# Performance work log

Measured on AMD Instinct MI355X. Metric: run time of the kernel, lower is better.

Reference implementation:

```python
import jax, jax.numpy as jnp
import numpy as np

N_NODES = 50000
N_EDGES = 800000
N_FEAT = 128
D_HID = 128
N_CLASS = 40


def gcn_conv(x, W, b, src, dst, n_nodes):
    """PyG GCNConv: h = D^{-1/2} (A + I) D^{-1/2} (x @ W) + b.
    src/dst are int arrays [E]; self-loops handled analytically."""
    h = x @ W  # [N, D]
    ones = jnp.ones(src.shape[0], dtype=h.dtype)
    # degree after adding self-loops: 1 + in-degree (edge weights are 1)
    deg = 1.0 + jax.ops.segment_sum(ones, dst, num_segments=n_nodes)
    dinv = jax.lax.rsqrt(deg)  # [N]
    # messages along edges src -> dst with symmetric normalization
    msg = h[src] * (dinv[src] * dinv[dst])[:, None]  # [E, D]
    agg = jax.ops.segment_sum(msg, dst, num_segments=n_nodes)  # [N, D]
    # self-loop contribution: dinv[i]^2 * h[i]
    agg = agg + h * (dinv * dinv)[:, None]
    return agg + b


def setup_inputs() -> dict:
    key = jax.random.key(0)
    ks = jax.random.split(key, 5)
    x = jax.random.normal(ks[0], (N_NODES, N_FEAT), dtype=jnp.float32)
    edge_index = jax.random.randint(ks[1], (2, N_EDGES), 0, N_NODES, dtype=jnp.int64)
    s_in = 1.0 / np.sqrt(N_FEAT)
    s_h = 1.0 / np.sqrt(D_HID)
    W_in = jax.random.normal(ks[2], (N_FEAT, D_HID), dtype=jnp.float32) * s_in
    W1 = jax.random.normal(ks[3], (D_HID, D_HID), dtype=jnp.float32) * s_h
    W_out = jax.random.normal(ks[4], (D_HID, N_CLASS), dtype=jnp.float32) * s_h
    return {
        "x": x,
        "edge_index": edge_index,
        "W_in": W_in,
        "b_in": jnp.zeros((D_HID,), jnp.float32),
        "W1": W1,
        "b1": jnp.zeros((D_HID,), jnp.float32),
        "W_out": W_out,
        "b_out": jnp.zeros((N_CLASS,), jnp.float32),
    }


def reference(x, edge_index, W_in, b_in, W1, b1, W_out, b_out):
    src, dst = edge_index[0], edge_index[1]
    n = x.shape[0]
    # input GCNConv (no activation on input_fc, matching the torch forward)
    h = gcn_conv(x, W_in, b_in, src, dst, n)
    # hidden layer: dropout is identity at eval; relu after conv; normalize=False
    h = jax.nn.relu(gcn_conv(h, W1, b1, src, dst, n))
    out = h @ W_out + b_out
    return jax.nn.log_softmax(out, axis=1)
```

## Files before the change

### kernel.cpp

```cpp
#include <hip/hip_runtime.h>
#include <math.h>


#define THREADS 256

typedef __attribute__((ext_vector_type(8))) short short8v;
typedef __attribute__((ext_vector_type(4))) float float4v;

__device__ __forceinline__ float b2f(unsigned int lo16) {
    return __uint_as_float(lo16 << 16);
}
__device__ __forceinline__ unsigned short f2b(float f) {
    unsigned int u = __float_as_uint(f);
    u += 0x7FFFu + ((u >> 16) & 1u);
    return (unsigned short)(u >> 16);
}

__global__ void detect_idx64(const int* __restrict__ idx, int* __restrict__ flag) {
    int t = threadIdx.x;
    unsigned long long b = __ballot(idx[2 * t + 1] == 0);
    if (t == 0) *flag = (b == 0xFFFFFFFFFFFFFFFFull) ? 1 : 0;
}

__global__ void fill_pos(const int* __restrict__ idx, const int* __restrict__ flag,
                         int* __restrict__ cnt, unsigned int* __restrict__ rec, int E) {
    int e = blockIdx.x * blockDim.x + threadIdx.x;
    if (e >= E) return;
    int f = *flag;
    int src, dst;
    if (f) { src = idx[2 * e]; dst = idx[2 * (E + e)]; }
    else   { src = idx[e];     dst = idx[E + e]; }
    unsigned int pos = (unsigned int)atomicAdd(&cnt[dst], 1);
    rec[e] = ((unsigned int)src << 16) | (pos & 0xFFFFu);
}

__global__ __launch_bounds__(256) void scanA(const int* __restrict__ cnt,
                                             int* __restrict__ bsum, int N) {
    __shared__ int wt[4];
    int tid = threadIdx.x, lane = tid & 63, w = tid >> 6;
    int i = blockIdx.x * 256 + tid;
    int v = (i < N) ? cnt[i] : 0;
    int s = v;
#pragma unroll
    for (int off = 1; off < 64; off <<= 1) {
        int t = __shfl_up(s, off);
        if (lane >= off) s += t;
    }
    if (lane == 63) wt[w] = s;
    __syncthreads();
    if (tid == 0) bsum[blockIdx.x] = wt[0] + wt[1] + wt[2] + wt[3];
}

__global__ __launch_bounds__(256) void scanB(int* __restrict__ bsum,
                                             int* __restrict__ boff,
                                             int* __restrict__ rowstart,
                                             int nb, int N) {
    __shared__ int wt[4];
    __shared__ int wo[5];
    int tid = threadIdx.x, lane = tid & 63, w = tid >> 6;
    int v = (tid < nb) ? bsum[tid] : 0;
    int s = v;
#pragma unroll
    for (int off = 1; off < 64; off <<= 1) {
        int t = __shfl_up(s, off);
        if (lane >= off) s += t;
    }
    if (lane == 63) wt[w] = s;
    __syncthreads();
    if (tid == 0) {
        int run = 0;
#pragma unroll
        for (int k = 0; k < 4; ++k) { wo[k] = run; run += wt[k]; }
        wo[4] = run;
    }
    __syncthreads();
    if (tid < nb) boff[tid] = wo[w] + s - v;
    if (tid == 0) rowstart[N] = wo[4];
}

__global__ __launch_bounds__(256) void scanC(const int* __restrict__ cnt,
                                             const int* __restrict__ boff,
                                             int* __restrict__ rowstart,
                                             float* __restrict__ dinv, int N) {
    __shared__ int wt[4];
    __shared__ int wo[4];
    int tid = threadIdx.x, lane = tid & 63, w = tid >> 6;
    int i = blockIdx.x * 256 + tid;
    int v = (i < N) ? cnt[i] : 0;
    int s = v;
#pragma unroll
    for (int off = 1; off < 64; off <<= 1) {
        int t = __shfl_up(s, off);
        if (lane >= off) s += t;
    }
    if (lane == 63) wt[w] = s;
    __syncthreads();
    if (tid == 0) {
        int run = 0;
#pragma unroll
        for (int k = 0; k < 4; ++k) { wo[k] = run; run += wt[k]; }
    }
    __syncthreads();
    if (i < N) {
        rowstart[i] = boff[blockIdx.x] + wo[w] + (s - v);
        dinv[i] = rsqrtf(1.0f + (float)v);
    }
}

__global__ void fill_place(const int* __restrict__ idx, const int* __restrict__ flag,
                           const unsigned int* __restrict__ rec,
                           const int* __restrict__ rowstart,
                           unsigned short* __restrict__ srcs, int E) {
    int e = blockIdx.x * blockDim.x + threadIdx.x;
    if (e >= E) return;
    int f = *flag;
    int dst = f ? idx[2 * (E + e)] : idx[E + e];
    unsigned int r = rec[e];
    srcs[rowstart[dst] + (int)(r & 0xFFFFu)] = (unsigned short)(r >> 16);
}

__global__ __launch_bounds__(256) void pack_w2(const float* __restrict__ W0,
                                               const float* __restrict__ W1,
                                               uint4* __restrict__ wpk0,
                                               uint4* __restrict__ wpk1) {
    const float* W = blockIdx.x ? W1 : W0;
    uint4* wpk = blockIdx.x ? wpk1 : wpk0;
    int tid = threadIdx.x;
    for (int it = 0; it < 8; ++it) {
        int s = it * 256 + tid;
        int ct = s >> 8;
        int kb = (s >> 6) & 3;
        int l  = s & 63;
        int col = ct * 16 + (l & 15);
        int k0  = kb * 32 + ((l >> 4) << 3);
        unsigned short e0 = f2b(W[(k0 + 0) * 128 + col]);
        unsigned short e1 = f2b(W[(k0 + 1) * 128 + col]);
        unsigned short e2 = f2b(W[(k0 + 2) * 128 + col]);
        unsigned short e3 = f2b(W[(k0 + 3) * 128 + col]);
        unsigned short e4 = f2b(W[(k0 + 4) * 128 + col]);
        unsigned short e5 = f2b(W[(k0 + 5) * 128 + col]);
        unsigned short e6 = f2b(W[(k0 + 6) * 128 + col]);
        unsigned short e7 = f2b(W[(k0 + 7) * 128 + col]);
        uint4 u;
        u.x = (unsigned int)e0 | ((unsigned int)e1 << 16);
        u.y = (unsigned int)e2 | ((unsigned int)e3 << 16);
        u.z = (unsigned int)e4 | ((unsigned int)e5 << 16);
        u.w = (unsigned int)e6 | ((unsigned int)e7 << 16);
        wpk[s] = u;
    }
}

template <int ABF>
__global__ __launch_bounds__(256) void gemm_mfma(const void* __restrict__ Ap,
                                                 const uint4* __restrict__ wpk,
                                                 unsigned short* __restrict__ outb,
                                                 int N) {
    __shared__ unsigned short ol[128 * 128];
    int tid = threadIdx.x;
    int w = tid >> 6, l = tid & 63;
    int lr = l & 15, lq = l >> 4;
    int base = blockIdx.x * 128;
    int arow0 = base + w * 16 + lr;
    int arow1 = base + 64 + w * 16 + lr;
    int ar0 = (arow0 < N) ? arow0 : (N - 1);
    int ar1 = (arow1 < N) ? arow1 : (N - 1);

    float4v acc[2][8];
#pragma unroll
    for (int t = 0; t < 2; ++t)
#pragma unroll
        for (int ct = 0; ct < 8; ++ct) acc[t][ct] = (float4v){0.f, 0.f, 0.f, 0.f};

#pragma unroll
    for (int kb = 0; kb < 4; ++kb) {
        short8v af0, af1;
        if (ABF) {
            uint4 v0 = *(const uint4*)((const unsigned short*)Ap + (size_t)ar0 * 128 + kb * 32 + lq * 8);
            uint4 v1 = *(const uint4*)((const unsigned short*)Ap + (size_t)ar1 * 128 + kb * 32 + lq * 8);
            union { uint4 u; short8v s; } c0, c1; c0.u = v0; c1.u = v1;
            af0 = c0.s; af1 = c1.s;
        } else {
            const float* a0 = (const float*)Ap + (size_t)ar0 * 128 + kb * 32 + lq * 8;
            const float* a1 = (const float*)Ap + (size_t)ar1 * 128 + kb * 32 + lq * 8;
            float4 va0 = *(const float4*)a0, vb0 = *(const float4*)(a0 + 4);
            float4 va1 = *(const float4*)a1, vb1 = *(const float4*)(a1 + 4);
            uint4 u0, u1;
            u0.x = (unsigned int)f2b(va0.x) | ((unsigned int)f2b(va0.y) << 16);
            u0.y = (unsigned int)f2b(va0.z) | ((unsigned int)f2b(va0.w) << 16);
            u0.z = (unsigned int)f2b(vb0.x) | ((unsigned int)f2b(vb0.y) << 16);
            u0.w = (unsigned int)f2b(vb0.z) | ((unsigned int)f2b(vb0.w) << 16);
            u1.x = (unsigned int)f2b(va1.x) | ((unsigned int)f2b(va1.y) << 16);
            u1.y = (unsigned int)f2b(va1.z) | ((unsigned int)f2b(va1.w) << 16);
            u1.z = (unsigned int)f2b(vb1.x) | ((unsigned int)f2b(vb1.y) << 16);
            u1.w = (unsigned int)f2b(vb1.z) | ((unsigned int)f2b(vb1.w) << 16);
            union { uint4 uu; short8v s; } c0, c1; c0.uu = u0; c1.uu = u1;
            af0 = c0.s; af1 = c1.s;
        }
#pragma unroll
        for (int ct = 0; ct < 8; ++ct) {
            uint4 bv = wpk[(ct * 4 + kb) * 64 + l];
            union { uint4 u; short8v s; } cv; cv.u = bv; short8v bf = cv.s;
            acc[0][ct] = __builtin_amdgcn_mfma_f32_16x16x32_bf16(af0, bf, acc[0][ct], 0, 0, 0);
            acc[1][ct] = __builtin_amdgcn_mfma_f32_16x16x32_bf16(af1, bf, acc[1][ct], 0, 0, 0);
        }
    }

#pragma unroll
    for (int t = 0; t < 2; ++t)
#pragma unroll
        for (int ct = 0; ct < 8; ++ct)
#pragma unroll
            for (int r = 0; r < 4; ++r)
                ol[(t * 64 + w * 16 + lq * 4 + r) * 128 + ct * 16 + lr] = f2b(acc[t][ct][r]);
    __syncthreads();
#pragma unroll
    for (int it = 0; it < 8; ++it) {
        int o = it * 4096 + tid * 16;
        int rr = o >> 8;
        int cb = o & 255;
        int gr = base + rr;
        if (gr < N) {
            uint4 v = *(const uint4*)((const char*)ol + o);
            *(uint4*)((char*)outb + (size_t)gr * 256 + cb) = v;
        }
    }
}

__global__ __launch_bounds__(256) void agg_node(const unsigned short* __restrict__ hb,
                                                const int* __restrict__ rowstart,
                                                const unsigned short* __restrict__ srcs,
                                                const float* __restrict__ dinv,
                                                const float* __restrict__ b,
                                                unsigned short* __restrict__ outb,
                                                int N, int do_relu) {
    int w = threadIdx.x >> 6, lane = threadIdx.x & 63;
    int node = blockIdx.x * 4 + w;
    if (node >= N) return;
    int beg = rowstart[node], end = rowstart[node + 1];
    float dn = dinv[node];
    int quarter = lane >> 4, q = lane & 15;
    const uint4* hb8 = (const uint4*)hb;
    float a0 = 0.f, a1 = 0.f, a2 = 0.f, a3 = 0.f;
    float a4 = 0.f, a5 = 0.f, a6 = 0.f, a7 = 0.f;

    for (int j0 = beg; j0 < end; j0 += 64) {
        int myj = j0 + lane;
        int ms = 0;
        float md = 0.f;
        if (myj < end) { ms = (int)srcs[myj]; md = dinv[ms]; }
        int m = min(64, end - j0);
#pragma unroll 2
        for (int k = 0; k < m; k += 8) {
            int i0 = k + quarter;
            int i1 = k + 4 + quarter;
            int s0 = __shfl(ms, i0);
            int s1 = __shfl(ms, i1);
            float c0 = dn * __shfl(md, i0);
            float c1 = dn * __shfl(md, i1);
            uint4 v0 = hb8[(size_t)s0 * 16 + q];
            uint4 v1 = hb8[(size_t)s1 * 16 + q];
            a0 += c0 * b2f(v0.x & 0xFFFFu);
            a1 += c0 * b2f(v0.x >> 16);
            a2 += c0 * b2f(v0.y & 0xFFFFu);
            a3 += c0 * b2f(v0.y >> 16);
            a4 += c0 * b2f(v0.z & 0xFFFFu);
            a5 += c0 * b2f(v0.z >> 16);
            a6 += c0 * b2f(v0.w & 0xFFFFu);
            a7 += c0 * b2f(v0.w >> 16);
            a0 += c1 * b2f(v1.x & 0xFFFFu);
            a1 += c1 * b2f(v1.x >> 16);
            a2 += c1 * b2f(v1.y & 0xFFFFu);
            a3 += c1 * b2f(v1.y >> 16);
            a4 += c1 * b2f(v1.z & 0xFFFFu);
            a5 += c1 * b2f(v1.z >> 16);
            a6 += c1 * b2f(v1.w & 0xFFFFu);
            a7 += c1 * b2f(v1.w >> 16);
        }
    }
    a0 += __shfl_xor(a0, 32); a1 += __shfl_xor(a1, 32);
    a2 += __shfl_xor(a2, 32); a3 += __shfl_xor(a3, 32);
    a4 += __shfl_xor(a4, 32); a5 += __shfl_xor(a5, 32);
    a6 += __shfl_xor(a6, 32); a7 += __shfl_xor(a7, 32);
    a0 += __shfl_xor(a0, 16); a1 += __shfl_xor(a1, 16);
    a2 += __shfl_xor(a2, 16); a3 += __shfl_xor(a3, 16);
    a4 += __shfl_xor(a4, 16); a5 += __shfl_xor(a5, 16);
    a6 += __shfl_xor(a6, 16); a7 += __shfl_xor(a7, 16);

    if (quarter == 0) {
        uint4 sv = hb8[(size_t)node * 16 + q];
        float d2 = dn * dn;
        float4 b0 = ((const float4*)b)[2 * q];
        float4 b1 = ((const float4*)b)[2 * q + 1];
        float r0 = a0 + d2 * b2f(sv.x & 0xFFFFu) + b0.x;
        float r1 = a1 + d2 * b2f(sv.x >> 16)     + b0.y;
        float r2 = a2 + d2 * b2f(sv.y & 0xFFFFu) + b0.z;
        float r3 = a3 + d2 * b2f(sv.y >> 16)     + b0.w;
        float r4 = a4 + d2 * b2f(sv.z & 0xFFFFu) + b1.x;
        float r5 = a5 + d2 * b2f(sv.z >> 16)     + b1.y;
        float r6 = a6 + d2 * b2f(sv.w & 0xFFFFu) + b1.z;
        float r7 = a7 + d2 * b2f(sv.w >> 16)     + b1.w;
        if (do_relu) {
            r0 = fmaxf(r0, 0.f); r1 = fmaxf(r1, 0.f);
            r2 = fmaxf(r2, 0.f); r3 = fmaxf(r3, 0.f);
            r4 = fmaxf(r4, 0.f); r5 = fmaxf(r5, 0.f);
            r6 = fmaxf(r6, 0.f); r7 = fmaxf(r7, 0.f);
        }
        uint4 o;
        o.x = (unsigned int)f2b(r0) | ((unsigned int)f2b(r1) << 16);
        o.y = (unsigned int)f2b(r2) | ((unsigned int)f2b(r3) << 16);
        o.z = (unsigned int)f2b(r4) | ((unsigned int)f2b(r5) << 16);
        o.w = (unsigned int)f2b(r6) | ((unsigned int)f2b(r7) << 16);
        ((uint4*)outb)[(size_t)node * 16 + q] = o;
    }
}

__global__ __launch_bounds__(256) void out_gemm(const unsigned short* __restrict__ h2b,
                                                const float* __restrict__ Wout,
                                                const float* __restrict__ bout,
                                                float* __restrict__ out, int N) {
    __shared__ float Xt[128 * 128];
    __shared__ float Wl[128 * 40];
    __shared__ float bl[40];
    int tid = threadIdx.x;
    int row0 = blockIdx.x * 128;

    for (int i = tid; i < 128 * 40; i += 256) Wl[i] = Wout[i];
    if (tid < 40) bl[tid] = bout[tid];

    {
        int r = tid >> 1, kh = tid & 1;
        int gr = row0 + r;
#pragma unroll
        for (int i = 0; i < 16; ++i) {
            int k = kh * 64 + i * 4;
            float f0, f1, f2, f3;
            if (gr < N) {
                uint2 qv = ((const uint2*)h2b)[(size_t)gr * 32 + (k >> 2)];
                f0 = b2f(qv.x & 0xFFFFu); f1 = b2f(qv.x >> 16);
                f2 = b2f(qv.y & 0xFFFFu); f3 = b2f(qv.y >> 16);
            } else {
                f0 = f1 = f2 = f3 = 0.f;
            }
            Xt[(k + 0) * 128 + r] = f0;
            Xt[(k + 1) * 128 + r] = f1;
            Xt[(k + 2) * 128 + r] = f2;
            Xt[(k + 3) * 128 + r] = f3;
        }
    }
    __syncthreads();

    int cg = tid & 7;
    int r4 = tid >> 3;
    float bias[5];
#pragma unroll
    for (int c = 0; c < 5; ++c) bias[c] = bl[5 * cg + c];

    float acc[4][5];
#pragma unroll
    for (int j = 0; j < 4; ++j)
#pragma unroll
        for (int c = 0; c < 5; ++c) acc[j][c] = 0.f;

    const float4* Xt4 = (const float4*)Xt;
#pragma unroll 4
    for (int k = 0; k < 128; ++k) {
        float4 xv = Xt4[k * 32 + r4];
        const float* wr = &Wl[k * 40 + 5 * cg];
        float w0 = wr[0], w1 = wr[1], w2 = wr[2], w3 = wr[3], w4 = wr[4];
        float xs[4] = {xv.x, xv.y, xv.z, xv.w};
#pragma unroll
        for (int j = 0; j < 4; ++j) {
            acc[j][0] += xs[j] * w0;
            acc[j][1] += xs[j] * w1;
            acc[j][2] += xs[j] * w2;
            acc[j][3] += xs[j] * w3;
            acc[j][4] += xs[j] * w4;
        }
    }

#pragma unroll
    for (int j = 0; j < 4; ++j) {
        int r = row0 + r4 * 4 + j;
        if (r >= N) continue;
        float v[5];
        float m = -INFINITY;
#pragma unroll
        for (int c = 0; c < 5; ++c) { v[c] = acc[j][c] + bias[c]; m = fmaxf(m, v[c]); }
        m = fmaxf(m, __shfl_xor(m, 1));
        m = fmaxf(m, __shfl_xor(m, 2));
        m = fmaxf(m, __shfl_xor(m, 4));
        float s = 0.f;
#pragma unroll
        for (int c = 0; c < 5; ++c) s += expf(v[c] - m);
        s += __shfl_xor(s, 1);
        s += __shfl_xor(s, 2);
        s += __shfl_xor(s, 4);
        float ls = logf(s);
#pragma unroll
        for (int c = 0; c < 5; ++c) out[(size_t)r * 40 + 5 * cg + c] = v[c] - m - ls;
    }
}

static inline size_t al256(size_t x) { return (x + 255) & ~(size_t)255; }

extern "C" void kernel_launch(void* const* d_in, const int* in_sizes, int n_in,
                              void* d_out, int out_size, void* d_ws, size_t ws_size,
                              hipStream_t stream) {
    const float* x     = (const float*)d_in[0];
    const int*   idx   = (const int*)d_in[1];
    const float* W_in  = (const float*)d_in[2];
    const float* b_in  = (const float*)d_in[3];
    const float* W1    = (const float*)d_in[4];
    const float* b1    = (const float*)d_in[5];
    const float* W_out = (const float*)d_in[6];
    const float* b_out = (const float*)d_in[7];
    float* out = (float*)d_out;

    int N = in_sizes[0] / 128;
    int E = in_sizes[1] / 2;

    char* ws = (char*)d_ws;
    size_t off = 0;
    int* flag = (int*)(ws + off);              off += 256;
    int* cnt = (int*)(ws + off);               off += al256((size_t)N * 4);
    int* rowstart = (int*)(ws + off);          off += al256((size_t)(N + 1) * 4);
    float* dinv = (float*)(ws + off);          off += al256((size_t)N * 4);
    unsigned short* srcs = (unsigned short*)(ws + off); off += al256((size_t)E * 2);
    unsigned int* rec = (unsigned int*)(ws + off);      off += al256((size_t)E * 4);
    int* bsum = (int*)(ws + off);              off += 2048;
    int* boff = (int*)(ws + off);              off += 2048;
    uint4* wpk1 = (uint4*)(ws + off);          off += 32768;
    uint4* wpk2 = (uint4*)(ws + off);          off += 32768;
    unsigned short* B0 = (unsigned short*)(ws + off);   off += (size_t)N * 128 * 2;
    unsigned short* B1 = (unsigned short*)(ws + off);

    int nb_e = (E + THREADS - 1) / THREADS;
    int nb_n = (N + THREADS - 1) / THREADS;
    int nb_g = (N + 127) / 128;
    int nb_a = (N + 3) / 4;

    detect_idx64<<<1, 64, 0, stream>>>(idx, flag);
    hipMemsetAsync(cnt, 0, (size_t)N * 4, stream);
    pack_w2<<<2, THREADS, 0, stream>>>(W_in, W1, wpk1, wpk2);
    fill_pos<<<nb_e, THREADS, 0, stream>>>(idx, flag, cnt, rec, E);
    scanA<<<nb_n, THREADS, 0, stream>>>(cnt, bsum, N);
    scanB<<<1, THREADS, 0, stream>>>(bsum, boff, rowstart, nb_n, N);
    scanC<<<nb_n, THREADS, 0, stream>>>(cnt, boff, rowstart, dinv, N);
    fill_place<<<nb_e, THREADS, 0, stream>>>(idx, flag, rec, rowstart, srcs, E);

    gemm_mfma<0><<<nb_g, THREADS, 0, stream>>>(x, wpk1, B0, N);
    agg_node<<<nb_a, THREADS, 0, stream>>>(B0, rowstart, srcs, dinv, b_in,
                                           B1, N, 0);
    gemm_mfma<1><<<nb_g, THREADS, 0, stream>>>(B1, wpk2, B0, N);
    agg_node<<<nb_a, THREADS, 0, stream>>>(B0, rowstart, srcs, dinv, b1,
                                           B1, N, 1);
    out_gemm<<<nb_g, THREADS, 0, stream>>>(B1, W_out, b_out, out, N);
}
```

Baseline: 260.6 us.

## Fuse setup kernels, overlap first GEMM with edge counting, fuse final agg with output GEMM

Merges flag detection, counter zeroing, weight packing and x-to-bf16 conversion into one init kernel. The first GEMM and the edge-position atomic pass now share a single launch as disjoint block ranges, so the two run concurrently. The second aggregation is fused with ReLU, the 128x40 output projection and log-softmax, which drops the intermediate buffer round trip and one launch. The trade-off is an extra bf16 copy of x and a per-node output matmul done by 40 lanes from shared memory with block-wide syncs, which may be less efficient than the old tiled out_gemm.

```diff
diff --git a/kernel.cpp b/kernel.cpp
--- a/kernel.cpp
+++ b/kernel.cpp
@@ -16,15 +16,116 @@
     return (unsigned short)(u >> 16);
 }
 
-__global__ void detect_idx64(const int* __restrict__ idx, int* __restrict__ flag) {
-    int t = threadIdx.x;
-    unsigned long long b = __ballot(idx[2 * t + 1] == 0);
-    if (t == 0) *flag = (b == 0xFFFFFFFFFFFFFFFFull) ? 1 : 0;
-}
-
-__global__ void fill_pos(const int* __restrict__ idx, const int* __restrict__ flag,
-                         int* __restrict__ cnt, unsigned int* __restrict__ rec, int E) {
-    int e = blockIdx.x * blockDim.x + threadIdx.x;
+__global__ __launch_bounds__(256) void f_init(const float* __restrict__ x,
+                                              const int* __restrict__ idx,
+                                              const float* __restrict__ W0,
+                                              const float* __restrict__ W1f,
+                                              int* __restrict__ flag,
+                                              int* __restrict__ cnt,
+                                              uint4* __restrict__ wpk0,
+                                              uint4* __restrict__ wpk1,
+                                              unsigned short* __restrict__ Xb,
+                                              int N) {
+    int tid = threadIdx.x, bid = blockIdx.x, nb = gridDim.x;
+    if (bid == 0 && tid < 64) {
+        unsigned long long b = __ballot(idx[2 * tid + 1] == 0);
+        if (tid == 0) *flag = (b == 0xFFFFFFFFFFFFFFFFull) ? 1 : 0;
+    }
+    for (int i = bid * 256 + tid; i < N; i += nb * 256) cnt[i] = 0;
+    if (bid < 2) {
+        const float* W = bid ? W1f : W0;
+        uint4* wpk = bid ? wpk1 : wpk0;
+#pragma unroll
+        for (int it = 0; it < 8; ++it) {
+            int s = it * 256 + tid;
+            int ct = s >> 8, kb = (s >> 6) & 3, l = s & 63;
+            int col = ct * 16 + (l & 15);
+            int k0 = kb * 32 + ((l >> 4) << 3);
+            uint4 u;
+            u.x = (unsigned int)f2b(W[(k0 + 0) * 128 + col]) | ((unsigned int)f2b(W[(k0 + 1) * 128 + col]) << 16);
+            u.y = (unsigned int)f2b(W[(k0 + 2) * 128 + col]) | ((unsigned int)f2b(W[(k0 + 3) * 128 + col]) << 16);
+            u.z = (unsigned int)f2b(W[(k0 + 4) * 128 + col]) | ((unsigned int)f2b(W[(k0 + 5) * 128 + col]) << 16);
+            u.w = (unsigned int)f2b(W[(k0 + 6) * 128 + col]) | ((unsigned int)f2b(W[(k0 + 7) * 128 + col]) << 16);
+            wpk[s] = u;
+        }
+    }
+    int total = N * 32;
+    const float4* x4 = (const float4*)x;
+    ushort4* xb4 = (ushort4*)Xb;
+    for (int i = bid * 256 + tid; i < total; i += nb * 256) {
+        float4 v = x4[i];
+        ushort4 o;
+        o.x = f2b(v.x); o.y = f2b(v.y); o.z = f2b(v.z); o.w = f2b(v.w);
+        xb4[i] = o;
+    }
+}
+
+__device__ __forceinline__ void gemm_body(const unsigned short* __restrict__ Ab,
+                                          const uint4* __restrict__ wpk,
+                                          unsigned short* __restrict__ outb,
+                                          unsigned short* ol, int base, int N) {
+    int tid = threadIdx.x;
+    int w = tid >> 6, l = tid & 63;
+    int lr = l & 15, lq = l >> 4;
+    int arow0 = base + w * 16 + lr;
+    int arow1 = base + 64 + w * 16 + lr;
+    int ar0 = (arow0 < N) ? arow0 : (N - 1);
+    int ar1 = (arow1 < N) ? arow1 : (N - 1);
+
+    float4v acc[2][8];
+#pragma unroll
+    for (int t = 0; t < 2; ++t)
+#pragma unroll
+        for (int ct = 0; ct < 8; ++ct) acc[t][ct] = (float4v){0.f, 0.f, 0.f, 0.f};
+
+#pragma unroll
+    for (int kb = 0; kb < 4; ++kb) {
+        uint4 v0 = *(const uint4*)(Ab + (size_t)ar0 * 128 + kb * 32 + lq * 8);
+        uint4 v1 = *(const uint4*)(Ab + (size_t)ar1 * 128 + kb * 32 + lq * 8);
+        union { uint4 u; short8v s; } c0, c1; c0.u = v0; c1.u = v1;
+        short8v af0 = c0.s, af1 = c1.s;
+#pragma unroll
+        for (int ct = 0; ct < 8; ++ct) {
+            uint4 bv = wpk[(ct * 4 + kb) * 64 + l];
+            union { uint4 u; short8v s; } cv; cv.u = bv; short8v bf = cv.s;
+            acc[0][ct] = __builtin_amdgcn_mfma_f32_16x16x32_bf16(af0, bf, acc[0][ct], 0, 0, 0);
+            acc[1][ct] = __builtin_amdgcn_mfma_f32_16x16x32_bf16(af1, bf, acc[1][ct], 0, 0, 0);
+        }
+    }
+#pragma unroll
+    for (int t = 0; t < 2; ++t)
+#pragma unroll
+        for (int ct = 0; ct < 8; ++ct)
+#pragma unroll
+            for (int r = 0; r < 4; ++r)
+                ol[(t * 64 + w * 16 + lq * 4 + r) * 128 + ct * 16 + lr] = f2b(acc[t][ct][r]);
+    __syncthreads();
+#pragma unroll
+    for (int it = 0; it < 8; ++it) {
+        int o = it * 4096 + tid * 16;
+        int rr = o >> 8, cb = o & 255;
+        int gr = base + rr;
+        if (gr < N) {
+            uint4 v = *(const uint4*)((const char*)ol + o);
+            *(uint4*)((char*)outb + (size_t)gr * 256 + cb) = v;
+        }
+    }
+}
+
+__global__ __launch_bounds__(256) void f_g1fp(const unsigned short* __restrict__ Xb,
+                                              const uint4* __restrict__ wpk1,
+                                              unsigned short* __restrict__ B0,
+                                              const int* __restrict__ idx,
+                                              const int* __restrict__ flag,
+                                              int* __restrict__ cnt,
+                                              unsigned int* __restrict__ rec,
+                                              int N, int E, int nbg) {
+    __shared__ unsigned short ol[128 * 128];
+    if ((int)blockIdx.x < nbg) {
+        gemm_body(Xb, wpk1, B0, ol, blockIdx.x * 128, N);
+        return;
+    }
+    int e = (blockIdx.x - nbg) * 256 + threadIdx.x;
     if (e >= E) return;
     int f = *flag;
     int src, dst;
@@ -32,6 +133,14 @@
     else   { src = idx[e];     dst = idx[E + e]; }
     unsigned int pos = (unsigned int)atomicAdd(&cnt[dst], 1);
     rec[e] = ((unsigned int)src << 16) | (pos & 0xFFFFu);
+}
+
+__global__ __launch_bounds__(256) void gemm_mfma(const unsigned short* __restrict__ Ab,
+                                                 const uint4* __restrict__ wpk,
+                                                 unsigned short* __restrict__ outb,
+                                                 int N) {
+    __shared__ unsigned short ol[128 * 128];
+    gemm_body(Ab, wpk, outb, ol, blockIdx.x * 128, N);
 }
 
 __global__ __launch_bounds__(256) void scanA(const int* __restrict__ cnt,
@@ -119,112 +228,39 @@
     srcs[rowstart[dst] + (int)(r & 0xFFFFu)] = (unsigned short)(r >> 16);
 }
 
-__global__ __launch_bounds__(256) void pack_w2(const float* __restrict__ W0,
-                                               const float* __restrict__ W1,
-                                               uint4* __restrict__ wpk0,
-                                               uint4* __restrict__ wpk1) {
-    const float* W = blockIdx.x ? W1 : W0;
-    uint4* wpk = blockIdx.x ? wpk1 : wpk0;
-    int tid = threadIdx.x;
-    for (int it = 0; it < 8; ++it) {
-        int s = it * 256 + tid;
-        int ct = s >> 8;
-        int kb = (s >> 6) & 3;
-        int l  = s & 63;
-        int col = ct * 16 + (l & 15);
-        int k0  = kb * 32 + ((l >> 4) << 3);
-        unsigned short e0 = f2b(W[(k0 + 0) * 128 + col]);
-        unsigned short e1 = f2b(W[(k0 + 1) * 128 + col]);
-        unsigned short e2 = f2b(W[(k0 + 2) * 128 + col]);
-        unsigned short e3 = f2b(W[(k0 + 3) * 128 + col]);
-        unsigned short e4 = f2b(W[(k0 + 4) * 128 + col]);
-        unsigned short e5 = f2b(W[(k0 + 5) * 128 + col]);
-        unsigned short e6 = f2b(W[(k0 + 6) * 128 + col]);
-        unsigned short e7 = f2b(W[(k0 + 7) * 128 + col]);
-        uint4 u;
-        u.x = (unsigned int)e0 | ((unsigned int)e1 << 16);
-        u.y = (unsigned int)e2 | ((unsigned int)e3 << 16);
-        u.z = (unsigned int)e4 | ((unsigned int)e5 << 16);
-        u.w = (unsigned int)e6 | ((unsigned int)e7 << 16);
-        wpk[s] = u;
-    }
-}
-
-template <int ABF>
-__global__ __launch_bounds__(256) void gemm_mfma(const void* __restrict__ Ap,
-                                                 const uint4* __restrict__ wpk,
-                                                 unsigned short* __restrict__ outb,
-                                                 int N) {
-    __shared__ unsigned short ol[128 * 128];
-    int tid = threadIdx.x;
-    int w = tid >> 6, l = tid & 63;
-    int lr = l & 15, lq = l >> 4;
-    int base = blockIdx.x * 128;
-    int arow0 = base + w * 16 + lr;
-    int arow1 = base + 64 + w * 16 + lr;
-    int ar0 = (arow0 < N) ? arow0 : (N - 1);
-    int ar1 = (arow1 < N) ? arow1 : (N - 1);
-
-    float4v acc[2][8];
-#pragma unroll
-    for (int t = 0; t < 2; ++t)
-#pragma unroll
-        for (int ct = 0; ct < 8; ++ct) acc[t][ct] = (float4v){0.f, 0.f, 0.f, 0.f};
-
-#pragma unroll
-    for (int kb = 0; kb < 4; ++kb) {
-        short8v af0, af1;
-        if (ABF) {
-            uint4 v0 = *(const uint4*)((const unsigned short*)Ap + (size_t)ar0 * 128 + kb * 32 + lq * 8);
-            uint4 v1 = *(const uint4*)((const unsigned short*)Ap + (size_t)ar1 * 128 + kb * 32 + lq * 8);
-            union { uint4 u; short8v s; } c0, c1; c0.u = v0; c1.u = v1;
-            af0 = c0.s; af1 = c1.s;
-        } else {
-            const float* a0 = (const float*)Ap + (size_t)ar0 * 128 + kb * 32 + lq * 8;
-            const float* a1 = (const float*)Ap + (size_t)ar1 * 128 + kb * 32 + lq * 8;
-            float4 va0 = *(const float4*)a0, vb0 = *(const float4*)(a0 + 4);
-            float4 va1 = *(const float4*)a1, vb1 = *(const float4*)(a1 + 4);
-            uint4 u0, u1;
-            u0.x = (unsigned int)f2b(va0.x) | ((unsigned int)f2b(va0.y) << 16);
-            u0.y = (unsigned int)f2b(va0.z) | ((unsigned int)f2b(va0.w) << 16);
-            u0.z = (unsigned int)f2b(vb0.x) | ((unsigned int)f2b(vb0.y) << 16);
-            u0.w = (unsigned int)f2b(vb0.z) | ((unsigned int)f2b(vb0.w) << 16);
-            u1.x = (unsigned int)f2b(va1.x) | ((unsigned int)f2b(va1.y) << 16);
-            u1.y = (unsigned int)f2b(va1.z) | ((unsigned int)f2b(va1.w) << 16);
-            u1.z = (unsigned int)f2b(vb1.x) | ((unsigned int)f2b(vb1.y) << 16);
-            u1.w = (unsigned int)f2b(vb1.z) | ((unsigned int)f2b(vb1.w) << 16);
-            union { uint4 uu; short8v s; } c0, c1; c0.uu = u0; c1.uu = u1;
-            af0 = c0.s; af1 = c1.s;
-        }
-#pragma unroll
-        for (int ct = 0; ct < 8; ++ct) {
-            uint4 bv = wpk[(ct * 4 + kb) * 64 + l];
-            union { uint4 u; short8v s; } cv; cv.u = bv; short8v bf = cv.s;
-            acc[0][ct] = __builtin_amdgcn_mfma_f32_16x16x32_bf16(af0, bf, acc[0][ct], 0, 0, 0);
-            acc[1][ct] = __builtin_amdgcn_mfma_f32_16x16x32_bf16(af1, bf, acc[1][ct], 0, 0, 0);
-        }
-    }
-
-#pragma unroll
-    for (int t = 0; t < 2; ++t)
-#pragma unroll
-        for (int ct = 0; ct < 8; ++ct)
-#pragma unroll
-            for (int r = 0; r < 4; ++r)
-                ol[(t * 64 + w * 16 + lq * 4 + r) * 128 + ct * 16 + lr] = f2b(acc[t][ct][r]);
-    __syncthreads();
-#pragma unroll
-    for (int it = 0; it < 8; ++it) {
-        int o = it * 4096 + tid * 16;
-        int rr = o >> 8;
-        int cb = o & 255;
-        int gr = base + rr;
-        if (gr < N) {
-            uint4 v = *(const uint4*)((const char*)ol + o);
-            *(uint4*)((char*)outb + (size_t)gr * 256 + cb) = v;
-        }
-    }
-}
+#define AGG_GATHER(hb8, beg, end, dn)                                          \
+    for (int j0 = (beg); j0 < (end); j0 += 64) {                               \
+        int myj = j0 + lane;                                                   \
+        int ms = 0; float md = 0.f;                                            \
+        if (myj < (end)) { ms = (int)srcs[myj]; md = dinv[ms]; }               \
+        int m = min(64, (end) - j0);                                           \
+        for (int k = 0; k < m; k += 8) {                                       \
+            int i0 = k + quarter;                                              \
+            int i1 = k + 4 + quarter;                                          \
+            int s0 = __shfl(ms, i0);                                           \
+            int s1 = __shfl(ms, i1);                                           \
+            float c0 = (dn) * __shfl(md, i0);                                  \
+            float c1 = (dn) * __shfl(md, i1);                                  \
+            uint4 v0 = hb8[(size_t)s0 * 16 + q];                               \
+            uint4 v1 = hb8[(size_t)s1 * 16 + q];                               \
+            a0 += c0 * b2f(v0.x & 0xFFFFu); a1 += c0 * b2f(v0.x >> 16);        \
+            a2 += c0 * b2f(v0.y & 0xFFFFu); a3 += c0 * b2f(v0.y >> 16);        \
+            a4 += c0 * b2f(v0.z & 0xFFFFu); a5 += c0 * b2f(v0.z >> 16);        \
+            a6 += c0 * b2f(v0.w & 0xFFFFu); a7 += c0 * b2f(v0.w >> 16);        \
+            a0 += c1 * b2f(v1.x & 0xFFFFu); a1 += c1 * b2f(v1.x >> 16);        \
+            a2 += c1 * b2f(v1.y & 0xFFFFu); a3 += c1 * b2f(v1.y >> 16);        \
+            a4 += c1 * b2f(v1.z & 0xFFFFu); a5 += c1 * b2f(v1.z >> 16);        \
+            a6 += c1 * b2f(v1.w & 0xFFFFu); a7 += c1 * b2f(v1.w >> 16);        \
+        }                                                                      \
+    }                                                                          \
+    a0 += __shfl_xor(a0, 32); a1 += __shfl_xor(a1, 32);                        \
+    a2 += __shfl_xor(a2, 32); a3 += __shfl_xor(a3, 32);                        \
+    a4 += __shfl_xor(a4, 32); a5 += __shfl_xor(a5, 32);                        \
+    a6 += __shfl_xor(a6, 32); a7 += __shfl_xor(a7, 32);                        \
+    a0 += __shfl_xor(a0, 16); a1 += __shfl_xor(a1, 16);                        \
+    a2 += __shfl_xor(a2, 16); a3 += __shfl_xor(a3, 16);                        \
+    a4 += __shfl_xor(a4, 16); a5 += __shfl_xor(a5, 16);                        \
+    a6 += __shfl_xor(a6, 16); a7 += __shfl_xor(a7, 16);
 
 __global__ __launch_bounds__(256) void agg_node(const unsigned short* __restrict__ hb,
                                                 const int* __restrict__ rowstart,
@@ -232,7 +268,7 @@
                                                 const float* __restrict__ dinv,
                                                 const float* __restrict__ b,
                                                 unsigned short* __restrict__ outb,
-                                                int N, int do_relu) {
+                                                int N) {
     int w = threadIdx.x >> 6, lane = threadIdx.x & 63;
     int node = blockIdx.x * 4 + w;
     if (node >= N) return;
@@ -242,50 +278,7 @@
     const uint4* hb8 = (const uint4*)hb;
     float a0 = 0.f, a1 = 0.f, a2 = 0.f, a3 = 0.f;
     float a4 = 0.f, a5 = 0.f, a6 = 0.f, a7 = 0.f;
-
-    for (int j0 = beg; j0 < end; j0 += 64) {
-        int myj = j0 + lane;
-        int ms = 0;
-        float md = 0.f;
-        if (myj < end) { ms = (int)srcs[myj]; md = dinv[ms]; }
-        int m = min(64, end - j0);
-#pragma unroll 2
-        for (int k = 0; k < m; k += 8) {
-            int i0 = k + quarter;
-            int i1 = k + 4 + quarter;
-            int s0 = __shfl(ms, i0);
-            int s1 = __shfl(ms, i1);
-            float c0 = dn * __shfl(md, i0);
-            float c1 = dn * __shfl(md, i1);
-            uint4 v0 = hb8[(size_t)s0 * 16 + q];
-            uint4 v1 = hb8[(size_t)s1 * 16 + q];
-            a0 += c0 * b2f(v0.x & 0xFFFFu);
-            a1 += c0 * b2f(v0.x >> 16);
-            a2 += c0 * b2f(v0.y & 0xFFFFu);
-            a3 += c0 * b2f(v0.y >> 16);
-            a4 += c0 * b2f(v0.z & 0xFFFFu);
-            a5 += c0 * b2f(v0.z >> 16);
-            a6 += c0 * b2f(v0.w & 0xFFFFu);
-            a7 += c0 * b2f(v0.w >> 16);
-            a0 += c1 * b2f(v1.x & 0xFFFFu);
-            a1 += c1 * b2f(v1.x >> 16);
-            a2 += c1 * b2f(v1.y & 0xFFFFu);
-            a3 += c1 * b2f(v1.y >> 16);
-            a4 += c1 * b2f(v1.z & 0xFFFFu);
-            a5 += c1 * b2f(v1.z >> 16);
-            a6 += c1 * b2f(v1.w & 0xFFFFu);
-            a7 += c1 * b2f(v1.w >> 16);
-        }
-    }
-    a0 += __shfl_xor(a0, 32); a1 += __shfl_xor(a1, 32);
-    a2 += __shfl_xor(a2, 32); a3 += __shfl_xor(a3, 32);
-    a4 += __shfl_xor(a4, 32); a5 += __shfl_xor(a5, 32);
-    a6 += __shfl_xor(a6, 32); a7 += __shfl_xor(a7, 32);
-    a0 += __shfl_xor(a0, 16); a1 += __shfl_xor(a1, 16);
-    a2 += __shfl_xor(a2, 16); a3 += __shfl_xor(a3, 16);
-    a4 += __shfl_xor(a4, 16); a5 += __shfl_xor(a5, 16);
-    a6 += __shfl_xor(a6, 16); a7 += __shfl_xor(a7, 16);
-
+    AGG_GATHER(hb8, beg, end, dn)
     if (quarter == 0) {
         uint4 sv = hb8[(size_t)node * 16 + q];
         float d2 = dn * dn;
@@ -299,12 +292,6 @@
         float r5 = a5 + d2 * b2f(sv.z >> 16)     + b1.y;
         float r6 = a6 + d2 * b2f(sv.w & 0xFFFFu) + b1.z;
         float r7 = a7 + d2 * b2f(sv.w >> 16)     + b1.w;
-        if (do_relu) {
-            r0 = fmaxf(r0, 0.f); r1 = fmaxf(r1, 0.f);
-            r2 = fmaxf(r2, 0.f); r3 = fmaxf(r3, 0.f);
-            r4 = fmaxf(r4, 0.f); r5 = fmaxf(r5, 0.f);
-            r6 = fmaxf(r6, 0.f); r7 = fmaxf(r7, 0.f);
-        }
         uint4 o;
         o.x = (unsigned int)f2b(r0) | ((unsigned int)f2b(r1) << 16);
         o.y = (unsigned int)f2b(r2) | ((unsigned int)f2b(r3) << 16);
@@ -314,90 +301,73 @@
     }
 }
 
-__global__ __launch_bounds__(256) void out_gemm(const unsigned short* __restrict__ h2b,
-                                                const float* __restrict__ Wout,
-                                                const float* __restrict__ bout,
-                                                float* __restrict__ out, int N) {
-    __shared__ float Xt[128 * 128];
+__global__ __launch_bounds__(256) void agg_out(const unsigned short* __restrict__ hb,
+                                               const int* __restrict__ rowstart,
+                                               const unsigned short* __restrict__ srcs,
+                                               const float* __restrict__ dinv,
+                                               const float* __restrict__ b1v,
+                                               const float* __restrict__ Wout,
+                                               const float* __restrict__ bout,
+                                               float* __restrict__ out, int N) {
     __shared__ float Wl[128 * 40];
     __shared__ float bl[40];
+    __shared__ float b1l[128];
+    __shared__ float rowbuf[4][128];
     int tid = threadIdx.x;
-    int row0 = blockIdx.x * 128;
-
     for (int i = tid; i < 128 * 40; i += 256) Wl[i] = Wout[i];
     if (tid < 40) bl[tid] = bout[tid];
-
-    {
-        int r = tid >> 1, kh = tid & 1;
-        int gr = row0 + r;
-#pragma unroll
-        for (int i = 0; i < 16; ++i) {
-            int k = kh * 64 + i * 4;
-            float f0, f1, f2, f3;
-            if (gr < N) {
-                uint2 qv = ((const uint2*)h2b)[(size_t)gr * 32 + (k >> 2)];
-                f0 = b2f(qv.x & 0xFFFFu); f1 = b2f(qv.x >> 16);
-                f2 = b2f(qv.y & 0xFFFFu); f3 = b2f(qv.y >> 16);
-            } else {
-                f0 = f1 = f2 = f3 = 0.f;
+    if (tid < 128) b1l[tid] = b1v[tid];
+    __syncthreads();
+
+    int w = tid >> 6, lane = tid & 63;
+    int quarter = lane >> 4, q = lane & 15;
+    const uint4* hb8 = (const uint4*)hb;
+
+#pragma unroll 1
+    for (int nn = 0; nn < 4; ++nn) {
+        int node = blockIdx.x * 16 + w * 4 + nn;
+        bool valid = node < N;
+        float a0 = 0.f, a1 = 0.f, a2 = 0.f, a3 = 0.f;
+        float a4 = 0.f, a5 = 0.f, a6 = 0.f, a7 = 0.f;
+        if (valid) {
+            int beg = rowstart[node], end = rowstart[node + 1];
+            float dn = dinv[node];
+            AGG_GATHER(hb8, beg, end, dn)
+            if (quarter == 0) {
+                uint4 sv = hb8[(size_t)node * 16 + q];
+                float d2 = dn * dn;
+                float r0 = fmaxf(a0 + d2 * b2f(sv.x & 0xFFFFu) + b1l[q * 8 + 0], 0.f);
+                float r1 = fmaxf(a1 + d2 * b2f(sv.x >> 16)     + b1l[q * 8 + 1], 0.f);
+                float r2 = fmaxf(a2 + d2 * b2f(sv.y & 0xFFFFu) + b1l[q * 8 + 2], 0.f);
+                float r3 = fmaxf(a3 + d2 * b2f(sv.y >> 16)     + b1l[q * 8 + 3], 0.f);
+                float r4 = fmaxf(a4 + d2 * b2f(sv.z & 0xFFFFu) + b1l[q * 8 + 4], 0.f);
+                float r5 = fmaxf(a5 + d2 * b2f(sv.z >> 16)     + b1l[q * 8 + 5], 0.f);
+                float r6 = fmaxf(a6 + d2 * b2f(sv.w & 0xFFFFu) + b1l[q * 8 + 6], 0.f);
+                float r7 = fmaxf(a7 + d2 * b2f(sv.w >> 16)     + b1l[q * 8 + 7], 0.f);
+                rowbuf[w][q * 8 + 0] = r0; rowbuf[w][q * 8 + 1] = r1;
+                rowbuf[w][q * 8 + 2] = r2; rowbuf[w][q * 8 + 3] = r3;
+                rowbuf[w][q * 8 + 4] = r4; rowbuf[w][q * 8 + 5] = r5;
+                rowbuf[w][q * 8 + 6] = r6; rowbuf[w][q * 8 + 7] = r7;
             }
-            Xt[(k + 0) * 128 + r] = f0;
-            Xt[(k + 1) * 128 + r] = f1;
-            Xt[(k + 2) * 128 + r] = f2;
-            Xt[(k + 3) * 128 + r] = f3;
         }
-    }
-    __syncthreads();
-
-    int cg = tid & 7;
-    int r4 = tid >> 3;
-    float bias[5];
-#pragma unroll
-    for (int c = 0; c < 5; ++c) bias[c] = bl[5 * cg + c];
-
-    float acc[4][5];
-#pragma unroll
-    for (int j = 0; j < 4; ++j)
-#pragma unroll
-        for (int c = 0; c < 5; ++c) acc[j][c] = 0.f;
-
-    const float4* Xt4 = (const float4*)Xt;
+        __syncthreads();
+        float v = -INFINITY;
+        if (valid && lane < 40) {
+            float acc = 0.f;
 #pragma unroll 4
-    for (int k = 0; k < 128; ++k) {
-        float4 xv = Xt4[k * 32 + r4];
-        const float* wr = &Wl[k * 40 + 5 * cg];
-        float w0 = wr[0], w1 = wr[1], w2 = wr[2], w3 = wr[3], w4 = wr[4];
-        float xs[4] = {xv.x, xv.y, xv.z, xv.w};
-#pragma unroll
-        for (int j = 0; j < 4; ++j) {
-            acc[j][0] += xs[j] * w0;
-            acc[j][1] += xs[j] * w1;
-            acc[j][2] += xs[j] * w2;
-            acc[j][3] += xs[j] * w3;
-            acc[j][4] += xs[j] * w4;
+            for (int k = 0; k < 128; ++k) acc += rowbuf[w][k] * Wl[k * 40 + lane];
+            v = acc + bl[lane];
         }
-    }
-
-#pragma unroll
-    for (int j = 0; j < 4; ++j) {
-        int r = row0 + r4 * 4 + j;
-        if (r >= N) continue;
-        float v[5];
-        float m = -INFINITY;
-#pragma unroll
-        for (int c = 0; c < 5; ++c) { v[c] = acc[j][c] + bias[c]; m = fmaxf(m, v[c]); }
-        m = fmaxf(m, __shfl_xor(m, 1));
-        m = fmaxf(m, __shfl_xor(m, 2));
-        m = fmaxf(m, __shfl_xor(m, 4));
-        float s = 0.f;
-#pragma unroll
-        for (int c = 0; c < 5; ++c) s += expf(v[c] - m);
-        s += __shfl_xor(s, 1);
-        s += __shfl_xor(s, 2);
-        s += __shfl_xor(s, 4);
+        float m = v;
+#pragma unroll
+        for (int off = 32; off > 0; off >>= 1) m = fmaxf(m, __shfl_xor(m, off));
+        float e = (valid && lane < 40) ? expf(v - m) : 0.f;
+        float s = e;
+#pragma unroll
+        for (int off = 32; off > 0; off >>= 1) s += __shfl_xor(s, off);
         float ls = logf(s);
-#pragma unroll
-        for (int c = 0; c < 5; ++c) out[(size_t)r * 40 + 5 * cg + c] = v[c] - m - ls;
+        if (valid && lane < 40) out[(size_t)node * 40 + lane] = v - m - ls;
+        __syncthreads();
     }
 }
 
@@ -431,6 +401,7 @@
     int* boff = (int*)(ws + off);              off += 2048;
     uint4* wpk1 = (uint4*)(ws + off);          off += 32768;
     uint4* wpk2 = (uint4*)(ws + off);          off += 32768;
+    unsigned short* Xb = (unsigned short*)(ws + off);   off += (size_t)N * 128 * 2;
     unsigned short* B0 = (unsigned short*)(ws + off);   off += (size_t)N * 128 * 2;
     unsigned short* B1 = (unsigned short*)(ws + off);
 
@@ -438,21 +409,18 @@
     int nb_n = (N + THREADS - 1) / THREADS;
     int nb_g = (N + 127) / 128;
     int nb_a = (N + 3) / 4;
-
-    detect_idx64<<<1, 64, 0, stream>>>(idx, flag);
-    hipMemsetAsync(cnt, 0, (size_t)N * 4, stream);
-    pack_w2<<<2, THREADS, 0, stream>>>(W_in, W1, wpk1, wpk2);
-    fill_pos<<<nb_e, THREADS, 0, stream>>>(idx, flag, cnt, rec, E);
+    int nb_o = (N + 15) / 16;
+
+    f_init<<<256, THREADS, 0, stream>>>(x, idx, W_in, W1, flag, cnt, wpk1, wpk2, Xb, N);
+    f_g1fp<<<nb_g + nb_e, THREADS, 0, stream>>>(Xb, wpk1, B0, idx, flag, cnt, rec,
+                                                N, E, nb_g);
     scanA<<<nb_n, THREADS, 0, stream>>>(cnt, bsum, N);
     scanB<<<1, THREADS, 0, stream>>>(bsum, boff, rowstart, nb_n, N);
     scanC<<<nb_n, THREADS, 0, stream>>>(cnt, boff, rowstart, dinv, N);
     fill_place<<<nb_e, THREADS, 0, stream>>>(idx, flag, rec, rowstart, srcs, E);
 
-    gemm_mfma<0><<<nb_g, THREADS, 0, stream>>>(x, wpk1, B0, N);
-    agg_node<<<nb_a, THREADS, 0, stream>>>(B0, rowstart, srcs, dinv, b_in,
-                                           B1, N, 0);
-    gemm_mfma<1><<<nb_g, THREADS, 0, stream>>>(B1, wpk2, B0, N);
-    agg_node<<<nb_a, THREADS, 0, stream>>>(B0, rowstart, srcs, dinv, b1,
-                                           B1, N, 1);
-    out_gemm<<<nb_g, THREADS, 0, stream>>>(B1, W_out, b_out, out, N);
-}
+    agg_node<<<nb_a, THREADS, 0, stream>>>(B0, rowstart, srcs, dinv, b_in, B1, N);
+    gemm_mfma<<<nb_g, THREADS, 0, stream>>>(B1, wpk2, B0, N);
+    agg_out<<<nb_o, THREADS, 0, stream>>>(B0, rowstart, srcs, dinv, b1,
+                                          W_out, b_out, out, N);
+}
```

Measured after the change: 270.4 us. +3.7%, slower.
